# Kernel optimization log

Hardware: AMD Instinct MI355X
Metric: run time of the kernel (lower is better)

Reference implementation:

```python
import jax, jax.numpy as jnp
import numpy as np

FEAT = 1433
HID = 2
NUM_CLASS = 7
EPS = 1e-5  # torch BatchNorm1d default eps


def _bn_softsign(h, gamma, beta):
    # BatchNorm1d in training mode: batch stats over (batch, length) per channel.
    mu = h.mean(axis=(0, 2), keepdims=True)
    var = h.var(axis=(0, 2), keepdims=True)  # biased, matches torch normalization
    hn = (h - mu) * jax.lax.rsqrt(var + EPS)
    hn = hn * gamma[None, :, None] + beta[None, :, None]
    return hn / (1.0 + jnp.abs(hn))  # Softsign


def feature_adjacency(x, y):
    # (x.unsqueeze(-1) * y.unsqueeze(-2)).sum(dim=1) with x channel dim == 1
    # reduces to an outer product of x[:,0] with neighbor.sum over K.
    adj = jnp.einsum('bf,bg->bfg', x.sum(1), y.sum(1))  # [B,F,F]
    adj = adj + jnp.swapaxes(adj, -1, -2)
    adj = jnp.sqrt(adj)
    # row_normalize: divide by sum over dim 1, zero out inf/nan
    norm = adj / adj.sum(axis=1, keepdims=True)
    norm = jnp.where(jnp.isfinite(norm), norm, 0.0)
    return norm + jnp.eye(FEAT, dtype=x.dtype)


def featbrd(x, adj, W, b):
    # adjacency-based feature conv: y[b,c,f] = sum_g adj[(b),f,g] x[b,c,g],
    # then 1x1 conv over channels (Conv1d kernel_size=1).
    if adj.shape[0] == 1:
        y = jnp.einsum('fg,bcg->bcf', adj[0], x)
    else:
        y = jnp.einsum('bfg,bcg->bcf', adj, x)
    return jnp.einsum('oc,bcf->bof', W, y) + b[None, :, None]


def setup_inputs() -> dict:
    key = jax.random.key(0)
    ks = jax.random.split(key, 10)
    B, K = 64, 8
    inp = {
        'x': jax.random.uniform(ks[0], (B, 1, FEAT), dtype=jnp.float32),
        'neighbor': jax.random.uniform(ks[1], (B, K, FEAT), dtype=jnp.float32),
        'adj_buf': jnp.zeros((1, FEAT, FEAT), jnp.float32),
        'W1': jax.random.normal(ks[2], (HID, 1), jnp.float32) * 0.5,
        'b1': jnp.zeros((HID,), jnp.float32),
        'W2': jax.random.normal(ks[3], (HID, HID), jnp.float32) * 0.5,
        'b2': jnp.zeros((HID,), jnp.float32),
        'g1': jnp.ones((HID,), jnp.float32),
        'be1': jnp.zeros((HID,), jnp.float32),
        'g2': jnp.ones((HID,), jnp.float32),
        'be2': jnp.zeros((HID,), jnp.float32),
        'Wc': jax.random.normal(ks[4], (NUM_CLASS, FEAT * HID), jnp.float32) * 0.02,
        'bc': jnp.zeros((NUM_CLASS,), jnp.float32),
    }
    return inp


def reference(x, neighbor, adj_buf, W1, b1, W2, b2, g1, be1, g2, be2, Wc, bc):
    fadj = feature_adjacency(x, neighbor)          # [B,F,F]
    adj_tot = adj_buf + fadj.sum(0)                # [1,F,F] (buffer starts at zero)
    h = _bn_softsign(featbrd(x, fadj, W1, b1), g1, be1)      # [B,HID,F]
    h = _bn_softsign(featbrd(h, adj_tot, W2, b2), g2, be2)   # [B,HID,F]
    flat = h.reshape(h.shape[0], -1)               # Flatten (C then F, row-major)
    return flat @ Wc.T + bc
```

## Files before the change

### kernel.cpp

```cpp
#include <hip/hip_runtime.h>
#include <hip/hip_bf16.h>
#include <math.h>

constexpr int F   = 1433;
constexpr int NB  = 64;
constexpr int KN  = 8;
constexpr int BF  = NB * F;
constexpr float EPS = 1e-5f;

constexpr int SF  = 16;
constexpr int CH  = 90;
constexpr int AbS = 1440;
constexpr int SK  = 9;
constexpr int FT  = 12;
constexpr int NA  = 720;
constexpr int NST = 256;

constexpr int O_YS  = 0;
constexpr int O_DP  = O_YS + BF;
constexpr int O_Y1P = O_DP + SF * BF;
constexpr int O_P   = O_Y1P + SF * BF;
constexpr int O_Y1  = O_P + 4 * BF;
constexpr int O_Y2  = O_Y1 + BF;
constexpr int O_G2P = O_Y2 + 2 * BF;
constexpr int O_AB  = O_G2P + SK * 128 * F;
constexpr int O_ST  = O_AB + (F * AbS) / 2;

__global__ __launch_bounds__(256) void k_ys(const float* __restrict__ nbr,
                                            float* __restrict__ ys,
                                            float* __restrict__ st) {
  const int b = blockIdx.x, q = blockIdx.y;
  if (b == 0 && q == 0 && threadIdx.x < 64) st[threadIdx.x] = 0.f;
  const int g = q * 256 + threadIdx.x;
  if (g < F) {
    const float* p = nbr + (size_t)b * KN * F + g;
    float a = 0.f;
#pragma unroll
    for (int k = 0; k < KN; ++k) a += p[k * F];
    ys[b * F + g] = a;
  }
}

__global__ __launch_bounds__(256) void k_D(const float* __restrict__ x,
                                           const float* __restrict__ ys,
                                           float* __restrict__ DP) {
  const int b = blockIdx.x, s = blockIdx.y;
  __shared__ __align__(8) float2 xyc[CH];
  const int cs = s * CH, cn = min(CH, F - cs);
  for (int i = threadIdx.x; i < cn; i += 256)
    xyc[i] = make_float2(x[b * F + cs + i], ys[b * F + cs + i]);
  __syncthreads();
  float gx[6], gy[6], acc[6] = {};
#pragma unroll
  for (int j = 0; j < 6; ++j) {
    int g = threadIdx.x + 256 * j;
    int gc = min(g, F - 1);
    gx[j] = (g < F) ? x[b * F + gc] : 0.f;
    gy[j] = (g < F) ? ys[b * F + gc] : 0.f;
  }
#pragma unroll 6
  for (int i = 0; i < cn; ++i) {
    float2 p = xyc[i];
#pragma unroll
    for (int j = 0; j < 6; ++j)
      acc[j] += __builtin_amdgcn_sqrtf(fmaf(gy[j], p.x, gx[j] * p.y));
  }
#pragma unroll
  for (int j = 0; j < 6; ++j) {
    int g = threadIdx.x + 256 * j;
    if (g < F) DP[(size_t)s * BF + b * F + g] = acc[j];
  }
}

__global__ __launch_bounds__(256) void k_y1(const float* __restrict__ x,
                                            const float* __restrict__ ys,
                                            const float* __restrict__ DP,
                                            float* __restrict__ Y1P,
                                            float4* __restrict__ P) {
  __shared__ __align__(16) float4 pl[CH];
  const int b = blockIdx.x, s = blockIdx.y;
  const int cs = s * CH, cn = min(CH, F - cs);
  for (int i = threadIdx.x; i < cn; i += 256) {
    int g = cs + i;
    float d = 0.f;
#pragma unroll
    for (int t = 0; t < SF; ++t) d += DP[(size_t)t * BF + b * F + g];
    float inv = (d > 0.f) ? 1.f / d : 0.f;
    float xv = x[b * F + g], yv = ys[b * F + g];
    float4 pv = make_float4(xv, yv, xv * inv, inv);
    pl[i] = pv;
    P[b * F + g] = pv;
  }
  __syncthreads();
  float fx[6], fy[6], acc[6] = {};
#pragma unroll
  for (int j = 0; j < 6; ++j) {
    int f = threadIdx.x + 256 * j;
    fx[j] = (f < F) ? x[b * F + f] : 0.f;
    fy[j] = (f < F) ? ys[b * F + f] : 0.f;
  }
#pragma unroll 6
  for (int i = 0; i < cn; ++i) {
    float4 p = pl[i];
#pragma unroll
    for (int j = 0; j < 6; ++j)
      acc[j] = fmaf(__builtin_amdgcn_sqrtf(fmaf(fx[j], p.y, fy[j] * p.x)), p.z, acc[j]);
  }
#pragma unroll
  for (int j = 0; j < 6; ++j) {
    int f = threadIdx.x + 256 * j;
    if (f < F) Y1P[(size_t)s * BF + b * F + f] = acc[j];
  }
}

__global__ __launch_bounds__(256) void k_Astats(const float* __restrict__ x,
                                                const float* __restrict__ ys,
                                                const float4* __restrict__ P,
                                                const float* __restrict__ Y1P,
                                                __hip_bfloat16* __restrict__ Ab,
                                                float* __restrict__ y1,
                                                float* __restrict__ st) {
  const int bid = blockIdx.x;
  if (bid < NA) {
    __shared__ float2 fxy[FT][NB];
    const int gxc = bid % 6, fy = bid / 6;
    const int fbase = fy * FT;
#pragma unroll
    for (int r = 0; r < 3; ++r) {
      int i = threadIdx.x + 256 * r;
      int j = i >> 6, bb = i & 63;
      int f = fbase + j;
      float vx = 0.f, vy = 0.f;
      if (f < F) { vx = x[bb * F + f]; vy = ys[bb * F + f]; }
      fxy[j][bb] = make_float2(vx, vy);
    }
    __syncthreads();
    const int g = gxc * 256 + threadIdx.x;
    if (g >= AbS) return;
    if (g < F) {
      float acc[FT] = {};
      float4 cur[4], nxt[4];
#pragma unroll
      for (int t = 0; t < 4; ++t) cur[t] = P[t * F + g];
      for (int bb = 0; bb < NB; bb += 4) {
        if (bb + 4 < NB) {
#pragma unroll
          for (int t = 0; t < 4; ++t) nxt[t] = P[(bb + 4 + t) * F + g];
        }
#pragma unroll
        for (int t = 0; t < 4; ++t) {
          float4 pc = cur[t];
#pragma unroll
          for (int j = 0; j < FT; ++j) {
            float2 w = fxy[j][bb + t];
            acc[j] = fmaf(__builtin_amdgcn_sqrtf(fmaf(w.x, pc.y, pc.x * w.y)), pc.w, acc[j]);
          }
        }
#pragma unroll
        for (int t = 0; t < 4; ++t) cur[t] = nxt[t];
      }
#pragma unroll
      for (int j = 0; j < FT; ++j) {
        int f = fbase + j;
        if (f < F) Ab[(size_t)f * AbS + g] = __float2bfloat16(acc[j]);
      }
    } else {
#pragma unroll
      for (int j = 0; j < FT; ++j) {
        int f = fbase + j;
        if (f < F) Ab[(size_t)f * AbS + g] = __float2bfloat16(0.f);
      }
    }
  } else {
    const int sid = bid - NA;
    float sv = 0.f, sq = 0.f;
    for (int i = sid * 256 + threadIdx.x; i < BF; i += NST * 256) {
      float v = x[i];
#pragma unroll
      for (int t = 0; t < SF; ++t) v += Y1P[(size_t)t * BF + i];
      y1[i] = v;
      sv += v; sq += v * v;
    }
#pragma unroll
    for (int o = 32; o; o >>= 1) {
      sv += __shfl_down(sv, o, 64);
      sq += __shfl_down(sq, o, 64);
    }
    __shared__ float ls[4], lq[4];
    int wave = threadIdx.x >> 6, lane = threadIdx.x & 63;
    if (lane == 0) { ls[wave] = sv; lq[wave] = sq; }
    __syncthreads();
    if (threadIdx.x == 0) {
      atomicAdd(&st[0], ls[0] + ls[1] + ls[2] + ls[3]);
      atomicAdd(&st[1], lq[0] + lq[1] + lq[2] + lq[3]);
    }
  }
}

__global__ __launch_bounds__(256, 4) void k_gemm(const ushort* __restrict__ Ab,
                                                 const float* __restrict__ y1,
                                                 const float* __restrict__ st,
                                                 const float* __restrict__ W1,
                                                 const float* __restrict__ g1,
                                                 const float* __restrict__ be1,
                                                 float* __restrict__ G2P) {
  const float mu = st[0] / (float)BF;
  const float var = st[1] / (float)BF - mu * mu;
  const float wa = W1[0], wb = W1[1];
  const float k0 = wa * g1[0] / sqrtf(wa * wa * var + EPS);
  const float k1 = wb * g1[1] / sqrtf(wb * wb * var + EPS);
  const float c0 = -k0 * mu + be1[0];
  const float c1 = -k1 * mu + be1[1];

  __shared__ __align__(16) float Al[32 * 36];
  __shared__ __align__(16) float Hl[32 * 132];
  const int f0 = blockIdx.x * 32;
  const int gs = blockIdx.y * 160;
  const int tid = threadIdx.x;
  const int ffs = tid >> 3, g4s = (tid & 7) * 4;
  const int hb = tid & 7, hg = tid >> 3;
  const int fsub = (tid & 7) * 4, msub = (tid >> 3) * 4;

  uint2 pa; float pyv[8];
  auto loadRegs = [&](int gb) {
    const int f = f0 + ffs;
    pa = make_uint2(0u, 0u);
    if (f < F) pa = *(const uint2*)&Ab[(size_t)f * AbS + gb + g4s];
    const int gl = min(gb + hg, F - 1);
#pragma unroll
    for (int r = 0; r < 8; ++r) pyv[r] = y1[(hb + 8 * r) * F + gl];
  };
  auto storeLDS = [&]() {
    Al[(g4s + 0) * 36 + ffs] = __uint_as_float(pa.x << 16);
    Al[(g4s + 1) * 36 + ffs] = __uint_as_float(pa.x & 0xffff0000u);
    Al[(g4s + 2) * 36 + ffs] = __uint_as_float(pa.y << 16);
    Al[(g4s + 3) * 36 + ffs] = __uint_as_float(pa.y & 0xffff0000u);
#pragma unroll
    for (int r = 0; r < 8; ++r) {
      const int bb = hb + 8 * r;
      const float v = pyv[r];
      float h0 = fmaf(k0, v, c0); h0 = h0 / (1.f + fabsf(h0));
      float h1 = fmaf(k1, v, c1); h1 = h1 / (1.f + fabsf(h1));
      *(float2*)&Hl[hg * 132 + 2 * bb] = make_float2(h0, h1);
    }
  };

  float acc[4][4] = {};
  loadRegs(gs);
  for (int c = 0; c < 5; ++c) {
    if (c) __syncthreads();
    storeLDS();
    __syncthreads();
    if (c < 4) loadRegs(gs + (c + 1) * 32);
#pragma unroll 4
    for (int gi = 0; gi < 32; ++gi) {
      float4 a4 = *(const float4*)&Al[gi * 36 + fsub];
      float4 h4 = *(const float4*)&Hl[gi * 132 + msub];
      float av[4] = {a4.x, a4.y, a4.z, a4.w};
      float hv[4] = {h4.x, h4.y, h4.z, h4.w};
#pragma unroll
      for (int i = 0; i < 4; ++i)
#pragma unroll
        for (int j = 0; j < 4; ++j)
          acc[i][j] = fmaf(av[i], hv[j], acc[i][j]);
    }
  }
  float* dst = G2P + (size_t)blockIdx.y * 128 * F;
#pragma unroll
  for (int i = 0; i < 4; ++i) {
    int f = f0 + fsub + i;
    if (f < F) {
#pragma unroll
      for (int j = 0; j < 4; ++j)
        dst[(msub + j) * F + f] = acc[i][j];
    }
  }
}

__global__ __launch_bounds__(256) void k_stats2(const float* __restrict__ y1,
                                                const float* __restrict__ G2P,
                                                const float* __restrict__ st,
                                                const float* __restrict__ W1,
                                                const float* __restrict__ g1,
                                                const float* __restrict__ be1,
                                                float* __restrict__ y2,
                                                float* __restrict__ stw) {
  const float mu = st[0] / (float)BF;
  const float var = st[1] / (float)BF - mu * mu;
  const float wa = W1[0], wb = W1[1];
  const float k0 = wa * g1[0] / sqrtf(wa * wa * var + EPS);
  const float k1 = wb * g1[1] / sqrtf(wb * wb * var + EPS);
  const float c0 = -k0 * mu + be1[0];
  const float c1 = -k1 * mu + be1[1];

  float su = 0.f, sv = 0.f, suu = 0.f, svv = 0.f, suv = 0.f;
  for (int i = blockIdx.x * 256 + threadIdx.x; i < BF; i += gridDim.x * 256) {
    int b = i / F, f = i - b * F;
    float w = y1[i];
    float h0 = fmaf(k0, w, c0); h0 = h0 / (1.f + fabsf(h0));
    float h1 = fmaf(k1, w, c1); h1 = h1 / (1.f + fabsf(h1));
    int iu = (2 * b) * F + f, iv = iu + F;
    float u = 64.f * h0, v = 64.f * h1;
#pragma unroll
    for (int t = 0; t < SK; ++t) {
      u += G2P[(size_t)t * 128 * F + iu];
      v += G2P[(size_t)t * 128 * F + iv];
    }
    y2[iu] = u; y2[iv] = v;
    su += u; sv += v; suu += u * u; svv += v * v; suv += u * v;
  }
#pragma unroll
  for (int o = 32; o; o >>= 1) {
    su += __shfl_down(su, o, 64);
    sv += __shfl_down(sv, o, 64);
    suu += __shfl_down(suu, o, 64);
    svv += __shfl_down(svv, o, 64);
    suv += __shfl_down(suv, o, 64);
  }
  __shared__ float red[5][4];
  int wave = threadIdx.x >> 6, lane = threadIdx.x & 63;
  if (lane == 0) {
    red[0][wave] = su; red[1][wave] = sv; red[2][wave] = suu;
    red[3][wave] = svv; red[4][wave] = suv;
  }
  __syncthreads();
  if (threadIdx.x == 0) {
#pragma unroll
    for (int m = 0; m < 5; ++m)
      atomicAdd(&stw[2 + m], red[m][0] + red[m][1] + red[m][2] + red[m][3]);
  }
}

__global__ __launch_bounds__(256) void k_out(const float* __restrict__ y2,
                                             const float* __restrict__ st,
                                             const float* __restrict__ W2,
                                             const float* __restrict__ b2,
                                             const float* __restrict__ g2,
                                             const float* __restrict__ be2,
                                             const float* __restrict__ Wc,
                                             const float* __restrict__ bc,
                                             float* __restrict__ out) {
  float n = (float)BF;
  float Eu = st[2] / n, Ev = st[3] / n;
  float Euu = st[4] / n, Evv = st[5] / n, Euv = st[6] / n;
  float cA[2], cB[2], cC[2];
#pragma unroll
  for (int o = 0; o < 2; ++o) {
    float w0 = W2[o * 2 + 0], w1 = W2[o * 2 + 1];
    float mean = w0 * Eu + w1 * Ev + b2[o];
    float Eh2 = w0 * w0 * Euu + 2.f * w0 * w1 * Euv + w1 * w1 * Evv +
                2.f * b2[o] * (w0 * Eu + w1 * Ev) + b2[o] * b2[o];
    float vr = Eh2 - mean * mean;
    float inv = g2[o] / sqrtf(vr + EPS);
    cA[o] = w0 * inv;
    cB[o] = w1 * inv;
    cC[o] = (b2[o] - mean) * inv + be2[o];
  }
  const int b = blockIdx.x;
  float acc[7] = {};
  for (int f = threadIdx.x; f < F; f += 256) {
    float u = y2[(2 * b) * F + f], v = y2[(2 * b + 1) * F + f];
    float h0 = fmaf(cA[0], u, fmaf(cB[0], v, cC[0]));
    h0 = h0 / (1.f + fabsf(h0));
    float h1 = fmaf(cA[1], u, fmaf(cB[1], v, cC[1]));
    h1 = h1 / (1.f + fabsf(h1));
#pragma unroll
    for (int o = 0; o < 7; ++o) acc[o] = fmaf(Wc[o * (2 * F) + f], h0, acc[o]);
#pragma unroll
    for (int o = 0; o < 7; ++o) acc[o] = fmaf(Wc[o * (2 * F) + F + f], h1, acc[o]);
  }
#pragma unroll
  for (int o = 0; o < 7; ++o) {
#pragma unroll
    for (int s = 32; s; s >>= 1) acc[o] += __shfl_down(acc[o], s, 64);
  }
  __shared__ float red[7][4];
  int wave = threadIdx.x >> 6, lane = threadIdx.x & 63;
  if (lane == 0) {
#pragma unroll
    for (int o = 0; o < 7; ++o) red[o][wave] = acc[o];
  }
  __syncthreads();
  if (threadIdx.x < 7) {
    int o = threadIdx.x;
    out[b * 7 + o] = red[o][0] + red[o][1] + red[o][2] + red[o][3] + bc[o];
  }
}

extern "C" void kernel_launch(void* const* d_in, const int* in_sizes, int n_in,
                              void* d_out, int out_size, void* d_ws, size_t ws_size,
                              hipStream_t stream) {
  const float* x    = (const float*)d_in[0];
  const float* nbr  = (const float*)d_in[1];
  const float* W1   = (const float*)d_in[3];
  const float* W2   = (const float*)d_in[5];
  const float* b2   = (const float*)d_in[6];
  const float* g1   = (const float*)d_in[7];
  const float* be1  = (const float*)d_in[8];
  const float* g2   = (const float*)d_in[9];
  const float* be2  = (const float*)d_in[10];
  const float* Wc   = (const float*)d_in[11];
  const float* bc   = (const float*)d_in[12];
  float* out = (float*)d_out;
  float* ws  = (float*)d_ws;

  float*  ys  = ws + O_YS;
  float*  DP  = ws + O_DP;
  float*  Y1P = ws + O_Y1P;
  float4* P   = (float4*)(ws + O_P);
  float*  y1  = ws + O_Y1;
  float*  y2  = ws + O_Y2;
  float*  G2P = ws + O_G2P;
  __hip_bfloat16* Ab = (__hip_bfloat16*)(ws + O_AB);
  float*  st  = ws + O_ST;

  k_ys    <<<dim3(NB, 6), 256, 0, stream>>>(nbr, ys, st);
  k_D     <<<dim3(NB, SF), 256, 0, stream>>>(x, ys, DP);
  k_y1    <<<dim3(NB, SF), 256, 0, stream>>>(x, ys, DP, Y1P, P);
  k_Astats<<<NA + NST, 256, 0, stream>>>(x, ys, P, Y1P, Ab, y1, st);
  k_gemm  <<<dim3(45, SK), 256, 0, stream>>>((const ushort*)Ab, y1, st, W1, g1, be1, G2P);
  k_stats2<<<NST, 256, 0, stream>>>(y1, G2P, st, W1, g1, be1, y2, st);
  k_out   <<<NB, 256, 0, stream>>>(y2, st, W2, b2, g2, be2, Wc, bc, out);
}
```

Measured before the change: 205.9 us.

## Exploit adjacency symmetry: compute upper-triangular tiles of summed adjacency once

The summed adjacency matrix is now built from 32x32 upper-triangular tiles. Each sqrt term is computed once and accumulated with two different row-normalisation weights, producing both the (f,g) and (g,f) entries. This is meant to roughly halve the sqrt and FMA work of building the matrix, and it moves per-batch parameters into shared memory. The GEMM's K-split is retuned from 9 to 15 chunks of 96 to keep that kernel's grid filled. The costs are a serial loop to map each block to its triangular tile and scattered bf16x4 writes for the transposed half.

```diff
diff --git a/kernel.cpp b/kernel.cpp
--- a/kernel.cpp
+++ b/kernel.cpp
@@ -11,9 +11,9 @@
 constexpr int SF  = 16;
 constexpr int CH  = 90;
 constexpr int AbS = 1440;
-constexpr int SK  = 9;
-constexpr int FT  = 12;
-constexpr int NA  = 720;
+constexpr int SK  = 15;
+constexpr int TP  = 45;
+constexpr int NTP = TP * (TP + 1) / 2;
 constexpr int NST = 256;
 
 constexpr int O_YS  = 0;
@@ -113,66 +113,64 @@
   }
 }
 
-__global__ __launch_bounds__(256) void k_Astats(const float* __restrict__ x,
-                                                const float* __restrict__ ys,
-                                                const float4* __restrict__ P,
-                                                const float* __restrict__ Y1P,
-                                                __hip_bfloat16* __restrict__ Ab,
-                                                float* __restrict__ y1,
-                                                float* __restrict__ st) {
+__global__ __launch_bounds__(256) void k_Asym(const float4* __restrict__ P,
+                                              const float* __restrict__ x,
+                                              const float* __restrict__ Y1P,
+                                              __hip_bfloat16* __restrict__ Ab,
+                                              float* __restrict__ y1,
+                                              float* __restrict__ st) {
   const int bid = blockIdx.x;
-  if (bid < NA) {
-    __shared__ float2 fxy[FT][NB];
-    const int gxc = bid % 6, fy = bid / 6;
-    const int fbase = fy * FT;
-#pragma unroll
-    for (int r = 0; r < 3; ++r) {
-      int i = threadIdx.x + 256 * r;
-      int j = i >> 6, bb = i & 63;
-      int f = fbase + j;
-      float vx = 0.f, vy = 0.f;
-      if (f < F) { vx = x[bb * F + f]; vy = ys[bb * F + f]; }
-      fxy[j][bb] = make_float2(vx, vy);
+  if (bid < NTP) {
+    int rem = bid, ti = 0;
+    while (rem >= TP - ti) { rem -= TP - ti; ++ti; }
+    const int tk = ti + rem;
+    const int fbase = ti * 32, gbase = tk * 32;
+    __shared__ __align__(16) float4 pf[NB][32];
+#pragma unroll
+    for (int r = 0; r < 8; ++r) {
+      int idx = threadIdx.x + 256 * r;
+      int bb = idx >> 5, fi = idx & 31;
+      int f = fbase + fi;
+      float4 v = make_float4(0.f, 0.f, 0.f, 0.f);
+      if (f < F) v = P[bb * F + f];
+      pf[bb][fi] = v;
     }
     __syncthreads();
-    const int g = gxc * 256 + threadIdx.x;
-    if (g >= AbS) return;
-    if (g < F) {
-      float acc[FT] = {};
-      float4 cur[4], nxt[4];
-#pragma unroll
-      for (int t = 0; t < 4; ++t) cur[t] = P[t * F + g];
-      for (int bb = 0; bb < NB; bb += 4) {
-        if (bb + 4 < NB) {
-#pragma unroll
-          for (int t = 0; t < 4; ++t) nxt[t] = P[(bb + 4 + t) * F + g];
-        }
-#pragma unroll
-        for (int t = 0; t < 4; ++t) {
-          float4 pc = cur[t];
-#pragma unroll
-          for (int j = 0; j < FT; ++j) {
-            float2 w = fxy[j][bb + t];
-            acc[j] = fmaf(__builtin_amdgcn_sqrtf(fmaf(w.x, pc.y, pc.x * w.y)), pc.w, acc[j]);
-          }
-        }
-#pragma unroll
-        for (int t = 0; t < 4; ++t) cur[t] = nxt[t];
+    const int g32 = threadIdx.x & 31, fq = threadIdx.x >> 5;
+    const int g = gbase + g32;
+    const bool gok = (g < F);
+    float4 cg = make_float4(0.f, 0.f, 0.f, 0.f), ng;
+    if (gok) cg = P[g];
+    float accA[4] = {}, accB[4] = {};
+    for (int b = 0; b < NB; ++b) {
+      ng = make_float4(0.f, 0.f, 0.f, 0.f);
+      if (gok && b + 1 < NB) ng = P[(b + 1) * F + g];
+      float4 pg = cg;
+#pragma unroll
+      for (int c = 0; c < 4; ++c) {
+        float4 pfv = pf[b][fq * 4 + c];
+        float s = __builtin_amdgcn_sqrtf(fmaf(pfv.x, pg.y, pg.x * pfv.y));
+        accA[c] = fmaf(s, pg.w, accA[c]);
+        accB[c] = fmaf(s, pfv.w, accB[c]);
       }
-#pragma unroll
-      for (int j = 0; j < FT; ++j) {
-        int f = fbase + j;
-        if (f < F) Ab[(size_t)f * AbS + g] = __float2bfloat16(acc[j]);
+      cg = ng;
+    }
+#pragma unroll
+    for (int c = 0; c < 4; ++c) {
+      int f = fbase + fq * 4 + c;
+      if (f < F) Ab[(size_t)f * AbS + g] = __float2bfloat16(accA[c]);
+    }
+    if (ti != tk && gok) {
+      union { ushort4 u; ushort h[4]; } pk;
+#pragma unroll
+      for (int c = 0; c < 4; ++c) {
+        __hip_bfloat16 hv = __float2bfloat16(accB[c]);
+        pk.h[c] = *reinterpret_cast<ushort*>(&hv);
       }
-    } else {
-#pragma unroll
-      for (int j = 0; j < FT; ++j) {
-        int f = fbase + j;
-        if (f < F) Ab[(size_t)f * AbS + g] = __float2bfloat16(0.f);
-      }
+      *reinterpret_cast<ushort4*>(&Ab[(size_t)g * AbS + fbase + fq * 4]) = pk.u;
     }
   } else {
-    const int sid = bid - NA;
+    const int sid = bid - NTP;
     float sv = 0.f, sq = 0.f;
     for (int i = sid * 256 + threadIdx.x; i < BF; i += NST * 256) {
       float v = x[i];
@@ -215,7 +213,7 @@
   __shared__ __align__(16) float Al[32 * 36];
   __shared__ __align__(16) float Hl[32 * 132];
   const int f0 = blockIdx.x * 32;
-  const int gs = blockIdx.y * 160;
+  const int gs = blockIdx.y * 96;
   const int tid = threadIdx.x;
   const int ffs = tid >> 3, g4s = (tid & 7) * 4;
   const int hb = tid & 7, hg = tid >> 3;
@@ -247,11 +245,11 @@
 
   float acc[4][4] = {};
   loadRegs(gs);
-  for (int c = 0; c < 5; ++c) {
+  for (int c = 0; c < 3; ++c) {
     if (c) __syncthreads();
     storeLDS();
     __syncthreads();
-    if (c < 4) loadRegs(gs + (c + 1) * 32);
+    if (c < 2) loadRegs(gs + (c + 1) * 32);
 #pragma unroll 4
     for (int gi = 0; gi < 32; ++gi) {
       float4 a4 = *(const float4*)&Al[gi * 36 + fsub];
@@ -417,7 +415,7 @@
   k_ys    <<<dim3(NB, 6), 256, 0, stream>>>(nbr, ys, st);
   k_D     <<<dim3(NB, SF), 256, 0, stream>>>(x, ys, DP);
   k_y1    <<<dim3(NB, SF), 256, 0, stream>>>(x, ys, DP, Y1P, P);
-  k_Astats<<<NA + NST, 256, 0, stream>>>(x, ys, P, Y1P, Ab, y1, st);
+  k_Asym  <<<NTP + NST, 256, 0, stream>>>(P, x, Y1P, Ab, y1, st);
   k_gemm  <<<dim3(45, SK), 256, 0, stream>>>((const ushort*)Ab, y1, st, W1, g1, be1, G2P);
   k_stats2<<<NST, 256, 0, stream>>>(y1, G2P, st, W1, g1, be1, y2, st);
   k_out   <<<NB, 256, 0, stream>>>(y2, st, W2, b2, g2, be2, Wc, bc, out);
```

New measurement: 218.7 us. +6.2%, slower.
